# Performance work log

Hardware: AMD Instinct MI355X
Metric: run time of the kernel (lower is better)

The kernel has to match this reference:

```python
import jax, jax.numpy as jnp
import numpy as np

B, S, D, H = 2, 2048, 1024, 16
HD = D // H  # head dim = 64


def setup_inputs() -> dict:
    key = jax.random.key(0)
    ks = jax.random.split(key, 5)
    scale = 0.02
    x = jax.random.normal(ks[0], (B, S, D), dtype=jnp.float32)
    Wqkv = jax.random.normal(ks[1], (D, 3 * D), dtype=jnp.float32) * scale
    bqkv = jnp.zeros((3 * D,), dtype=jnp.float32)
    Wproj = jax.random.normal(ks[2], (D, D), dtype=jnp.float32) * scale
    bproj = jnp.zeros((D,), dtype=jnp.float32)
    return {"x": x, "Wqkv": Wqkv, "bqkv": bqkv, "Wproj": Wproj, "bproj": bproj}


def reference(x, Wqkv, bqkv, Wproj, bproj):
    # fused QKV projection
    qkv = x @ Wqkv + bqkv                      # [B, S, 3D]
    q, k, v = jnp.split(qkv, 3, axis=-1)       # each [B, S, D]
    # split heads -> [B, H, S, HD]
    def heads(t):
        return t.reshape(B, S, H, HD).transpose(0, 2, 1, 3)
    q, k, v = heads(q), heads(k), heads(v)
    # scaled dot-product attention with causal mask (GPT-2 style)
    scores = jnp.einsum('bhqd,bhkd->bhqk', q, k) / jnp.sqrt(jnp.float32(HD))
    causal = jnp.tril(jnp.ones((S, S), dtype=bool))
    scores = jnp.where(causal, scores, jnp.finfo(scores.dtype).min)
    attn = jax.nn.softmax(scores, axis=-1)      # [B, H, S, S]
    out = jnp.einsum('bhqk,bhkd->bhqd', attn, v)  # [B, H, S, HD]
    out = out.transpose(0, 2, 1, 3).reshape(B, S, D)
    return out @ Wproj + bproj
```

## Files before the change

kernel.cpp:

```cpp
#include <hip/hip_runtime.h>
#include <hip/hip_bf16.h>


typedef __attribute__((ext_vector_type(8))) short short8;
typedef __attribute__((ext_vector_type(4))) float float4v;

#define S_LEN 2048
#define NHEAD 16
#define HDIM  64
#define DMODEL 1024

__device__ __forceinline__ unsigned short f2bf(float f) {
    union { float f; unsigned u; } v; v.f = f;
    unsigned r = v.u + 0x7FFF + ((v.u >> 16) & 1);
    return (unsigned short)(r >> 16);
}

__device__ __forceinline__ unsigned fbits_rn(float f) {
    union { float f; unsigned u; } v; v.f = f;
    return v.u + 0x8000u;
}

__device__ __forceinline__ void async16(const void* g, const void* l) {
    __builtin_amdgcn_global_load_lds(
        (const __attribute__((address_space(1))) unsigned int*)g,
        (__attribute__((address_space(3))) unsigned int*)l, 16, 0, 0);
}

__global__ void f32_to_bf16_v4(const float4* __restrict__ in,
                               ushort4* __restrict__ out, int n4) {
    int i = blockIdx.x * blockDim.x + threadIdx.x;
    if (i < n4) {
        float4 v = in[i];
        ushort4 o;
        o.x = f2bf(v.x); o.y = f2bf(v.y); o.z = f2bf(v.z); o.w = f2bf(v.w);
        out[i] = o;
    }
}

__global__ __launch_bounds__(256) void w_transpose_bf16(
    const float* __restrict__ Wqkv, const float* __restrict__ Wproj,
    unsigned short* __restrict__ outQ, unsigned short* __restrict__ outP) {
    __shared__ float t[64][65];
    const float* in; unsigned short* out; int N, bxl;
    if (blockIdx.x < 48) { in = Wqkv;  out = outQ; N = 3072; bxl = blockIdx.x; }
    else                 { in = Wproj; out = outP; N = 1024; bxl = blockIdx.x - 48; }
    const int K = 1024;
    const int kb = blockIdx.y * 64, nb = bxl * 64;
    const int tid = threadIdx.x;
    const int r0 = tid >> 4, c0 = (tid & 15) * 4;
#pragma unroll
    for (int g = 0; g < 4; g++) {
        float4 v = *(const float4*)(in + (size_t)(kb + g * 16 + r0) * N + nb + c0);
        t[g * 16 + r0][c0 + 0] = v.x; t[g * 16 + r0][c0 + 1] = v.y;
        t[g * 16 + r0][c0 + 2] = v.z; t[g * 16 + r0][c0 + 3] = v.w;
    }
    __syncthreads();
#pragma unroll
    for (int g = 0; g < 4; g++) {
        int n = g * 16 + r0;
        ushort4 o;
        o.x = f2bf(t[c0 + 0][n]); o.y = f2bf(t[c0 + 1][n]);
        o.z = f2bf(t[c0 + 2][n]); o.w = f2bf(t[c0 + 3][n]);
        *(ushort4*)(out + (size_t)(nb + n) * K + kb + c0) = o;
    }
}

__global__ __launch_bounds__(256) void v_transpose_sw(
    const unsigned short* __restrict__ V, unsigned short* __restrict__ Vt) {
    __shared__ unsigned short t[64 * 68];
    const int bh = blockIdx.y;
    const int s0 = blockIdx.x * 64;
    const int tid = threadIdx.x;
    const int r = tid >> 2;
    const int c4 = tid & 3;
    const size_t base = (size_t)bh * S_LEN * HDIM;
    union { uint4 v[2]; unsigned short u[16]; } d;
    const unsigned short* src = V + base + (size_t)(s0 + r) * HDIM + c4 * 16;
    d.v[0] = *(const uint4*)(src);
    d.v[1] = *(const uint4*)(src + 8);
#pragma unroll
    for (int j = 0; j < 16; j++) t[(c4 * 16 + j) * 68 + r] = d.u[j];
    __syncthreads();
    const int h4 = r & 15;
    const unsigned short* pl = t + r * 68 + c4 * 16;
    unsigned short* po = Vt + base + (size_t)r * S_LEN + s0
                         + (((c4 * 4) ^ (h4 & 12)) << 2);
    uint2 ug[4];
#pragma unroll
    for (int i = 0; i < 4; i++)
        ug[i ^ (h4 & 3)] = *(const uint2*)(pl + i * 4);
    uint4 w0; w0.x = ug[0].x; w0.y = ug[0].y; w0.z = ug[1].x; w0.w = ug[1].y;
    uint4 w1; w1.x = ug[2].x; w1.y = ug[2].y; w1.z = ug[3].x; w1.w = ug[3].y;
    *(uint4*)(po) = w0;
    *(uint4*)(po + 8) = w1;
}

#define QSCALE 0.18033688f

__global__ __launch_bounds__(256) void gemm_qkv_kernel(
    const unsigned short* __restrict__ A,
    const unsigned short* __restrict__ Bt,
    const float* __restrict__ bias,
    unsigned short* __restrict__ out_q,
    unsigned short* __restrict__ out_k,
    unsigned short* __restrict__ out_v,
    int M, int N, int K)
{
    __shared__ unsigned short smem[128 * 132];
    unsigned short* As = smem;
    unsigned short* Bs = smem + 128 * 32;

    const int tid  = threadIdx.x;
    const int lane = tid & 63;
    const int wave = tid >> 6;
    const int quad = lane >> 4;
    const int l16  = lane & 15;

    const int m0 = blockIdx.y * 128;
    const int n0 = blockIdx.x * 128;
    const int wm = (wave >> 1) * 64;
    const int wn = (wave & 1) * 64;

    float4v acc[4][4];
#pragma unroll
    for (int i = 0; i < 4; i++)
#pragma unroll
        for (int j = 0; j < 4; j++) acc[i][j] = (float4v){0.f, 0.f, 0.f, 0.f};

    const int srow = lane >> 2;
    const int scol = (lane & 3) * 8;

    for (int k0 = 0; k0 < K; k0 += 32) {
        __syncthreads();
#pragma unroll
        for (int it = 0; it < 2; it++) {
            const int rg = it * 64 + wave * 16;
            async16(A  + (size_t)(m0 + rg + srow) * K + k0 + scol,
                    (const char*)As + rg * 64);
            async16(Bt + (size_t)(n0 + rg + srow) * K + k0 + scol,
                    (const char*)Bs + rg * 64);
        }
        __syncthreads();

        short8 af[4], bf[4];
#pragma unroll
        for (int mt = 0; mt < 4; mt++)
            af[mt] = *(const short8*)(As + (wm + mt * 16 + l16) * 32 + quad * 8);
#pragma unroll
        for (int nt = 0; nt < 4; nt++)
            bf[nt] = *(const short8*)(Bs + (wn + nt * 16 + l16) * 32 + quad * 8);
#pragma unroll
        for (int mt = 0; mt < 4; mt++)
#pragma unroll
            for (int nt = 0; nt < 4; nt++)
                acc[mt][nt] = __builtin_amdgcn_mfma_f32_16x16x32_bf16(
                    af[mt], bf[nt], acc[mt][nt], 0, 0, 0);
    }

    __syncthreads();
#pragma unroll
    for (int nt = 0; nt < 4; nt++) {
        const int col = n0 + wn + nt * 16 + l16;
        const float sc = ((col >> 10) == 0) ? QSCALE : 1.0f;
        const float bia = bias[col] * sc;
        const int cold = (wn + nt * 16 + l16) >> 1;
#pragma unroll
        for (int mt = 0; mt < 4; mt++)
#pragma unroll
            for (int r = 0; r < 4; r++) {
                unsigned fb = fbits_rn(acc[mt][nt][r] * sc + bia);
                unsigned fbp = (unsigned)__shfl_xor((int)fb, 1, 64);
                unsigned pd = (l16 & 1)
                    ? __builtin_amdgcn_perm(fb, fbp, 0x07060302)
                    : __builtin_amdgcn_perm(fbp, fb, 0x07060302);
                const int rowl = wm + mt * 16 + quad * 4 + r;
                *((unsigned*)smem + rowl * 66 + cold) = pd;
            }
    }
    __syncthreads();

#pragma unroll
    for (int ps = 0; ps < 8; ps++) {
        const int row = ps * 16 + (tid >> 4);
        const int pc  = tid & 15;
        const int col0 = pc * 8;
        const int haf = col0 >> 6;
        const int cb = n0 + haf * 64;
        const int part = cb >> 10;
        const int h = (cb & 1023) >> 6;
        const int gr = m0 + row;
        const int b = gr >> 11, s = gr & 2047;
        const size_t bhI = (size_t)(b * NHEAD + h);
        const unsigned short* pl = smem + row * 132 + col0;
        uint2 a = *(const uint2*)(pl);
        uint2 bb = *(const uint2*)(pl + 4);
        uint4 w; w.x = a.x; w.y = a.y; w.z = bb.x; w.w = bb.y;
        unsigned short* po;
        if (part == 1) {
            const int plane = (col0 & 63) >> 5;
            po = out_k + ((bhI * 2 + plane) * S_LEN + s) * 32 + (col0 & 31);
        } else {
            unsigned short* dst = (part == 0) ? out_q : out_v;
            po = dst + (bhI * S_LEN + s) * HDIM + (col0 & 63);
        }
        *(uint4*)po = w;
    }
}

__global__ __launch_bounds__(256) void gemm_proj_kernel(
    const unsigned short* __restrict__ A,
    const unsigned short* __restrict__ Bt,
    const float* __restrict__ bias,
    float* __restrict__ out_f,
    int M, int N, int K)
{
    __shared__ unsigned short smem[(64 + 128) * 32];
    unsigned short* As = smem;
    unsigned short* Bs = smem + 64 * 32;

    const int tid  = threadIdx.x;
    const int lane = tid & 63;
    const int wave = tid >> 6;
    const int quad = lane >> 4;
    const int l16  = lane & 15;

    const int m0 = blockIdx.y * 64;
    const int n0 = blockIdx.x * 128;
    const int wm = (wave >> 1) * 32;
    const int wn = (wave & 1) * 64;

    float4v acc[2][4];
#pragma unroll
    for (int i = 0; i < 2; i++)
#pragma unroll
        for (int j = 0; j < 4; j++) acc[i][j] = (float4v){0.f, 0.f, 0.f, 0.f};

    const int srow = lane >> 2;
    const int scol = (lane & 3) * 8;

    for (int k0 = 0; k0 < K; k0 += 32) {
        __syncthreads();
        async16(A + (size_t)(m0 + wave * 16 + srow) * K + k0 + scol,
                (const char*)As + wave * 1024);
#pragma unroll
        for (int it = 0; it < 2; it++) {
            const int rg = it * 64 + wave * 16;
            async16(Bt + (size_t)(n0 + rg + srow) * K + k0 + scol,
                    (const char*)Bs + rg * 64);
        }
        __syncthreads();

        short8 af[2], bf[4];
#pragma unroll
        for (int mt = 0; mt < 2; mt++)
            af[mt] = *(const short8*)(As + (wm + mt * 16 + l16) * 32 + quad * 8);
#pragma unroll
        for (int nt = 0; nt < 4; nt++)
            bf[nt] = *(const short8*)(Bs + (wn + nt * 16 + l16) * 32 + quad * 8);
#pragma unroll
        for (int mt = 0; mt < 2; mt++)
#pragma unroll
            for (int nt = 0; nt < 4; nt++)
                acc[mt][nt] = __builtin_amdgcn_mfma_f32_16x16x32_bf16(
                    af[mt], bf[nt], acc[mt][nt], 0, 0, 0);
    }

#pragma unroll
    for (int nt = 0; nt < 4; nt++) {
        const int col = n0 + wn + nt * 16 + l16;
        const float bia = bias[col];
#pragma unroll
        for (int mt = 0; mt < 2; mt++) {
            const int rowb = m0 + wm + mt * 16 + quad * 4;
#pragma unroll
            for (int r = 0; r < 4; r++)
                out_f[(size_t)(rowb + r) * N + col] = acc[mt][nt][r] + bia;
        }
    }
}

__device__ __forceinline__ void attn_stage(
    const unsigned short* __restrict__ K2, const unsigned short* __restrict__ Vt,
    unsigned short* __restrict__ Ks, unsigned short* __restrict__ Vs,
    size_t baseK, size_t baseV, int kb0, int wave, int lane)
{
#pragma unroll
    for (int it = 0; it < 2; it++)
        async16(K2 + baseK + ((size_t)it * S_LEN + kb0 + wave * 16 + (lane >> 2)) * 32
                    + (lane & 3) * 8,
                (const char*)(Ks + (it * 64 + wave * 16) * 32));
#pragma unroll
    for (int it = 0; it < 2; it++)
        async16(Vt + baseV + (size_t)(it * 32 + wave * 8 + (lane >> 3)) * S_LEN
                    + kb0 + (lane & 7) * 8,
                (const char*)(Vs + (it * 32 + wave * 8) * 64));
}

__global__ __launch_bounds__(256) void attn3_kernel(
    const unsigned short* __restrict__ Q,
    const unsigned short* __restrict__ K2,
    const unsigned short* __restrict__ Vt,
    unsigned short* __restrict__ ctx)
{
    __shared__ unsigned short Ks[2][128 * 32];
    __shared__ unsigned short Vs[2][64 * 64];

    const int tid  = threadIdx.x;
    const int lane = tid & 63;
    const int wave = tid >> 6;
    const int quad = lane >> 4;
    const int l16  = lane & 15;

    const int bx = blockIdx.x;
    const int bh = bx & 31;
    const int qb = 31 - (bx >> 5);
    const int q0 = qb * 64 + wave * 16;
    const int nch = qb + 1;

    const size_t baseQ = (size_t)bh * S_LEN * HDIM;
    const size_t baseK = (size_t)bh * 2 * S_LEN * 32;
    const size_t baseV = (size_t)bh * HDIM * S_LEN;

    short8 qf[2];
#pragma unroll
    for (int h = 0; h < 2; h++)
        qf[h] = *(const short8*)(Q + baseQ + (size_t)(q0 + l16) * HDIM
                                 + h * 32 + quad * 8);

    float4v o[4];
#pragma unroll
    for (int nt = 0; nt < 4; nt++) o[nt] = (float4v){0.f, 0.f, 0.f, 0.f};
    float lsum = 0.f;

    attn_stage(K2, Vt, Ks[0], Vs[0], baseK, baseV, 0, wave, lane);

    for (int c = 0; c < nch; c++) {
        const int buf = c & 1;
        __syncthreads();
        if (c + 1 < nch)
            attn_stage(K2, Vt, Ks[buf ^ 1], Vs[buf ^ 1],
                       baseK, baseV, (c + 1) * 64, wave, lane);

        const int kb0 = c * 64;
        short8 kf[4][2];
#pragma unroll
        for (int kt = 0; kt < 4; kt++)
#pragma unroll
            for (int h = 0; h < 2; h++)
                kf[kt][h] = *(const short8*)&Ks[buf][(h * 64 + kt * 16 + l16) * 32
                                                     + quad * 8];
        float4v st[4];
#pragma unroll
        for (int kt = 0; kt < 4; kt++) {
            st[kt] = __builtin_amdgcn_mfma_f32_16x16x32_bf16(
                kf[kt][0], qf[0], (float4v){0.f, 0.f, 0.f, 0.f}, 0, 0, 0);
            st[kt] = __builtin_amdgcn_mfma_f32_16x16x32_bf16(
                kf[kt][1], qf[1], st[kt], 0, 0, 0);
        }
        const bool lastc = (c == nch - 1);
        const int qpos = q0 + l16;
        float p[4][4];
#pragma unroll
        for (int kt = 0; kt < 4; kt++)
#pragma unroll
            for (int r = 0; r < 4; r++) {
                float x = st[kt][r];
                if (lastc) {
                    int kpos = kb0 + kt * 16 + quad * 4 + r;
                    x = (kpos <= qpos) ? x : -1e30f;
                }
                p[kt][r] = __builtin_amdgcn_exp2f(x);
                lsum += p[kt][r];
            }

        unsigned pk[4][2];
#pragma unroll
        for (int kt = 0; kt < 4; kt++)
#pragma unroll
            for (int j = 0; j < 2; j++)
                pk[kt][j] = __builtin_amdgcn_perm(
                    fbits_rn(p[kt][2 * j + 1]), fbits_rn(p[kt][2 * j]),
                    0x07060302);
        union { unsigned u[4]; short8 s; } pf[2];
#pragma unroll
        for (int kk = 0; kk < 2; kk++)
#pragma unroll
            for (int pp = 0; pp < 4; pp++)
                pf[kk].u[pp] = pk[kk * 2 + (pp >> 1)][pp & 1];

#pragma unroll
        for (int nt = 0; nt < 4; nt++) {
            union { ushort4 h[2]; short8 s; } vf[2];
#pragma unroll
            for (int kt = 0; kt < 4; kt++)
                vf[kt >> 1].h[kt & 1] = *(const ushort4*)&Vs[buf][
                    (nt * 16 + l16) * 64 + (((kt * 4 + quad) ^ l16) << 2)];
            o[nt] = __builtin_amdgcn_mfma_f32_16x16x32_bf16(
                pf[0].s, vf[0].s, o[nt], 0, 0, 0);
            o[nt] = __builtin_amdgcn_mfma_f32_16x16x32_bf16(
                pf[1].s, vf[1].s, o[nt], 0, 0, 0);
        }
    }

    float l = lsum;
    l += __shfl_xor(l, 16, 64);
    l += __shfl_xor(l, 32, 64);
    const float linv = 1.f / l;
    float lr[4];
#pragma unroll
    for (int r = 0; r < 4; r++) lr[r] = __shfl(linv, quad * 4 + r, 64);

    const int b = bh >> 4, h = bh & 15;
#pragma unroll
    for (int r = 0; r < 4; r++) {
        const int s = q0 + quad * 4 + r;
        const size_t off = ((size_t)(b * S_LEN + s)) * DMODEL + h * HDIM;
#pragma unroll
        for (int nt = 0; nt < 4; nt++)
            ctx[off + nt * 16 + l16] = f2bf(o[nt][r] * lr[r]);
    }
}

extern "C" void kernel_launch(void* const* d_in, const int* in_sizes, int n_in,
                              void* d_out, int out_size, void* d_ws, size_t ws_size,
                              hipStream_t stream) {
    const float* x     = (const float*)d_in[0];
    const float* Wqkv  = (const float*)d_in[1];
    const float* bqkv  = (const float*)d_in[2];
    const float* Wproj = (const float*)d_in[3];
    const float* bproj = (const float*)d_in[4];
    float* out = (float*)d_out;

    const int M  = 2 * S_LEN;
    const int N1 = 3 * DMODEL;
    const int K  = DMODEL;

    unsigned short* x_bf    = (unsigned short*)d_ws;
    unsigned short* wqkv_t  = x_bf   + (size_t)M * K;
    unsigned short* wproj_t = wqkv_t + (size_t)K * N1;
    unsigned short* q_bf    = wproj_t + (size_t)K * DMODEL;
    unsigned short* k_bf    = q_bf   + (size_t)M * DMODEL;
    unsigned short* v_bf    = k_bf   + (size_t)M * DMODEL;
    unsigned short* ctx_bf  = v_bf   + (size_t)M * DMODEL;
    unsigned short* vt_bf   = x_bf;

    {
        int n4 = (M * K) / 4;
        f32_to_bf16_v4<<<n4 / 256, 256, 0, stream>>>((const float4*)x,
                                                     (ushort4*)x_bf, n4);
    }
    {
        dim3 g(64, 16);
        w_transpose_bf16<<<g, 256, 0, stream>>>(Wqkv, Wproj, wqkv_t, wproj_t);
    }

    dim3 g1(N1 / 128, M / 128);
    gemm_qkv_kernel<<<g1, 256, 0, stream>>>(x_bf, wqkv_t, bqkv,
                                            q_bf, k_bf, v_bf, M, N1, K);

    {
        dim3 g(S_LEN / 64, 2 * NHEAD);
        v_transpose_sw<<<g, 256, 0, stream>>>(v_bf, vt_bf);
    }

    attn3_kernel<<<1024, 256, 0, stream>>>(q_bf, k_bf, vt_bf, ctx_bf);

    dim3 g3(DMODEL / 128, M / 64);
    gemm_proj_kernel<<<g3, 256, 0, stream>>>(ctx_bf, wproj_t, bproj, out,
                                             M, DMODEL, K);
}
```

Baseline: 195.6 us.

## Deepen GEMM K-step to 64 and enlarge attention query blocks to 128

Both GEMM kernels now load two 32-wide K slices per barrier pair, so each iteration runs twice as many MFMAs between syncs and the number of synchronisations is halved. The attention kernel moves to 512-thread blocks covering 128 query rows, with 8 waves sharing each K/V tile. The query-block order is rescheduled to alternate heavy and light blocks, and causal masking is applied to any chunk overlapping the diagonal rather than only the last one. This aims to cut barrier overhead and increase K/V reuse per load, at the cost of more LDS per GEMM block and fewer, larger attention blocks.

```diff
diff --git a/kernel.cpp b/kernel.cpp
--- a/kernel.cpp
+++ b/kernel.cpp
@@ -109,7 +109,7 @@
 {
     __shared__ unsigned short smem[128 * 132];
     unsigned short* As = smem;
-    unsigned short* Bs = smem + 128 * 32;
+    unsigned short* Bs = smem + 8192;
 
     const int tid  = threadIdx.x;
     const int lane = tid & 63;
@@ -131,31 +131,38 @@
     const int srow = lane >> 2;
     const int scol = (lane & 3) * 8;
 
-    for (int k0 = 0; k0 < K; k0 += 32) {
+    for (int k0 = 0; k0 < K; k0 += 64) {
         __syncthreads();
 #pragma unroll
-        for (int it = 0; it < 2; it++) {
-            const int rg = it * 64 + wave * 16;
-            async16(A  + (size_t)(m0 + rg + srow) * K + k0 + scol,
-                    (const char*)As + rg * 64);
-            async16(Bt + (size_t)(n0 + rg + srow) * K + k0 + scol,
-                    (const char*)Bs + rg * 64);
-        }
+        for (int kk = 0; kk < 2; kk++)
+#pragma unroll
+            for (int it = 0; it < 2; it++) {
+                const int rg = it * 64 + wave * 16;
+                async16(A  + (size_t)(m0 + rg + srow) * K + k0 + kk * 32 + scol,
+                        (const char*)(As + kk * 4096) + rg * 64);
+                async16(Bt + (size_t)(n0 + rg + srow) * K + k0 + kk * 32 + scol,
+                        (const char*)(Bs + kk * 4096) + rg * 64);
+            }
         __syncthreads();
 
-        short8 af[4], bf[4];
-#pragma unroll
-        for (int mt = 0; mt < 4; mt++)
-            af[mt] = *(const short8*)(As + (wm + mt * 16 + l16) * 32 + quad * 8);
-#pragma unroll
-        for (int nt = 0; nt < 4; nt++)
-            bf[nt] = *(const short8*)(Bs + (wn + nt * 16 + l16) * 32 + quad * 8);
-#pragma unroll
-        for (int mt = 0; mt < 4; mt++)
+#pragma unroll
+        for (int kk = 0; kk < 2; kk++) {
+            short8 af[4], bf[4];
+#pragma unroll
+            for (int mt = 0; mt < 4; mt++)
+                af[mt] = *(const short8*)(As + kk * 4096
+                                          + (wm + mt * 16 + l16) * 32 + quad * 8);
 #pragma unroll
             for (int nt = 0; nt < 4; nt++)
-                acc[mt][nt] = __builtin_amdgcn_mfma_f32_16x16x32_bf16(
-                    af[mt], bf[nt], acc[mt][nt], 0, 0, 0);
+                bf[nt] = *(const short8*)(Bs + kk * 4096
+                                          + (wn + nt * 16 + l16) * 32 + quad * 8);
+#pragma unroll
+            for (int mt = 0; mt < 4; mt++)
+#pragma unroll
+                for (int nt = 0; nt < 4; nt++)
+                    acc[mt][nt] = __builtin_amdgcn_mfma_f32_16x16x32_bf16(
+                        af[mt], bf[nt], acc[mt][nt], 0, 0, 0);
+        }
     }
 
     __syncthreads();
@@ -215,9 +222,9 @@
     float* __restrict__ out_f,
     int M, int N, int K)
 {
-    __shared__ unsigned short smem[(64 + 128) * 32];
+    __shared__ unsigned short smem[12288];
     unsigned short* As = smem;
-    unsigned short* Bs = smem + 64 * 32;
+    unsigned short* Bs = smem + 4096;
 
     const int tid  = threadIdx.x;
     const int lane = tid & 63;
@@ -239,31 +246,39 @@
     const int srow = lane >> 2;
     const int scol = (lane & 3) * 8;
 
-    for (int k0 = 0; k0 < K; k0 += 32) {
+    for (int k0 = 0; k0 < K; k0 += 64) {
         __syncthreads();
-        async16(A + (size_t)(m0 + wave * 16 + srow) * K + k0 + scol,
-                (const char*)As + wave * 1024);
-#pragma unroll
-        for (int it = 0; it < 2; it++) {
-            const int rg = it * 64 + wave * 16;
-            async16(Bt + (size_t)(n0 + rg + srow) * K + k0 + scol,
-                    (const char*)Bs + rg * 64);
+#pragma unroll
+        for (int kk = 0; kk < 2; kk++) {
+            async16(A + (size_t)(m0 + wave * 16 + srow) * K + k0 + kk * 32 + scol,
+                    (const char*)(As + kk * 2048) + wave * 1024);
+#pragma unroll
+            for (int it = 0; it < 2; it++) {
+                const int rg = it * 64 + wave * 16;
+                async16(Bt + (size_t)(n0 + rg + srow) * K + k0 + kk * 32 + scol,
+                        (const char*)(Bs + kk * 4096) + rg * 64);
+            }
         }
         __syncthreads();
 
-        short8 af[2], bf[4];
-#pragma unroll
-        for (int mt = 0; mt < 2; mt++)
-            af[mt] = *(const short8*)(As + (wm + mt * 16 + l16) * 32 + quad * 8);
-#pragma unroll
-        for (int nt = 0; nt < 4; nt++)
-            bf[nt] = *(const short8*)(Bs + (wn + nt * 16 + l16) * 32 + quad * 8);
-#pragma unroll
-        for (int mt = 0; mt < 2; mt++)
+#pragma unroll
+        for (int kk = 0; kk < 2; kk++) {
+            short8 af[2], bf[4];
+#pragma unroll
+            for (int mt = 0; mt < 2; mt++)
+                af[mt] = *(const short8*)(As + kk * 2048
+                                          + (wm + mt * 16 + l16) * 32 + quad * 8);
 #pragma unroll
             for (int nt = 0; nt < 4; nt++)
-                acc[mt][nt] = __builtin_amdgcn_mfma_f32_16x16x32_bf16(
-                    af[mt], bf[nt], acc[mt][nt], 0, 0, 0);
+                bf[nt] = *(const short8*)(Bs + kk * 4096
+                                          + (wn + nt * 16 + l16) * 32 + quad * 8);
+#pragma unroll
+            for (int mt = 0; mt < 2; mt++)
+#pragma unroll
+                for (int nt = 0; nt < 4; nt++)
+                    acc[mt][nt] = __builtin_amdgcn_mfma_f32_16x16x32_bf16(
+                        af[mt], bf[nt], acc[mt][nt], 0, 0, 0);
+        }
     }
 
 #pragma unroll
@@ -280,24 +295,7 @@
     }
 }
 
-__device__ __forceinline__ void attn_stage(
-    const unsigned short* __restrict__ K2, const unsigned short* __restrict__ Vt,
-    unsigned short* __restrict__ Ks, unsigned short* __restrict__ Vs,
-    size_t baseK, size_t baseV, int kb0, int wave, int lane)
-{
-#pragma unroll
-    for (int it = 0; it < 2; it++)
-        async16(K2 + baseK + ((size_t)it * S_LEN + kb0 + wave * 16 + (lane >> 2)) * 32
-                    + (lane & 3) * 8,
-                (const char*)(Ks + (it * 64 + wave * 16) * 32));
-#pragma unroll
-    for (int it = 0; it < 2; it++)
-        async16(Vt + baseV + (size_t)(it * 32 + wave * 8 + (lane >> 3)) * S_LEN
-                    + kb0 + (lane & 7) * 8,
-                (const char*)(Vs + (it * 32 + wave * 8) * 64));
-}
-
-__global__ __launch_bounds__(256) void attn3_kernel(
+__global__ __launch_bounds__(512) void attn4_kernel(
     const unsigned short* __restrict__ Q,
     const unsigned short* __restrict__ K2,
     const unsigned short* __restrict__ Vt,
@@ -314,14 +312,20 @@
 
     const int bx = blockIdx.x;
     const int bh = bx & 31;
-    const int qb = 31 - (bx >> 5);
-    const int q0 = qb * 64 + wave * 16;
-    const int nch = qb + 1;
+    const int j  = bx >> 5;
+    const int qb = (j < 8) ? (15 - j) : (j - 8);
+    const int q0 = qb * 128 + wave * 16;
+    const int nch = 2 * qb + 2;
 
     const size_t baseQ = (size_t)bh * S_LEN * HDIM;
     const size_t baseK = (size_t)bh * 2 * S_LEN * 32;
     const size_t baseV = (size_t)bh * HDIM * S_LEN;
 
+    const int krw = wave * 16 + (lane >> 2);
+    const int kcol = (lane & 3) * 8;
+    const int vrw = wave * 8 + (lane >> 3);
+    const int vcol = (lane & 7) * 8;
+
     short8 qf[2];
 #pragma unroll
     for (int h = 0; h < 2; h++)
@@ -333,14 +337,21 @@
     for (int nt = 0; nt < 4; nt++) o[nt] = (float4v){0.f, 0.f, 0.f, 0.f};
     float lsum = 0.f;
 
-    attn_stage(K2, Vt, Ks[0], Vs[0], baseK, baseV, 0, wave, lane);
+#define ATTN_STAGE(buf, kb0)                                                   \
+    do {                                                                       \
+        async16(K2 + baseK + ((size_t)(krw >> 6) * S_LEN + (kb0) + (krw & 63)) \
+                    * 32 + kcol,                                               \
+                (const char*)Ks[buf] + wave * 1024);                           \
+        async16(Vt + baseV + (size_t)vrw * S_LEN + (kb0) + vcol,               \
+                (const char*)Vs[buf] + wave * 1024);                           \
+    } while (0)
+
+    ATTN_STAGE(0, 0);
 
     for (int c = 0; c < nch; c++) {
         const int buf = c & 1;
         __syncthreads();
-        if (c + 1 < nch)
-            attn_stage(K2, Vt, Ks[buf ^ 1], Vs[buf ^ 1],
-                       baseK, baseV, (c + 1) * 64, wave, lane);
+        if (c + 1 < nch) ATTN_STAGE(buf ^ 1, (c + 1) * 64);
 
         const int kb0 = c * 64;
         short8 kf[4][2];
@@ -358,7 +369,7 @@
             st[kt] = __builtin_amdgcn_mfma_f32_16x16x32_bf16(
                 kf[kt][1], qf[1], st[kt], 0, 0, 0);
         }
-        const bool lastc = (c == nch - 1);
+        const bool needm = (kb0 + 63 > q0);
         const int qpos = q0 + l16;
         float p[4][4];
 #pragma unroll
@@ -366,7 +377,7 @@
 #pragma unroll
             for (int r = 0; r < 4; r++) {
                 float x = st[kt][r];
-                if (lastc) {
+                if (needm) {
                     int kpos = kb0 + kt * 16 + quad * 4 + r;
                     x = (kpos <= qpos) ? x : -1e30f;
                 }
@@ -378,9 +389,9 @@
 #pragma unroll
         for (int kt = 0; kt < 4; kt++)
 #pragma unroll
-            for (int j = 0; j < 2; j++)
-                pk[kt][j] = __builtin_amdgcn_perm(
-                    fbits_rn(p[kt][2 * j + 1]), fbits_rn(p[kt][2 * j]),
+            for (int jj = 0; jj < 2; jj++)
+                pk[kt][jj] = __builtin_amdgcn_perm(
+                    fbits_rn(p[kt][2 * jj + 1]), fbits_rn(p[kt][2 * jj]),
                     0x07060302);
         union { unsigned u[4]; short8 s; } pf[2];
 #pragma unroll
@@ -402,6 +413,7 @@
                 pf[1].s, vf[1].s, o[nt], 0, 0, 0);
         }
     }
+#undef ATTN_STAGE
 
     float l = lsum;
     l += __shfl_xor(l, 16, 64);
@@ -464,7 +476,7 @@
         v_transpose_sw<<<g, 256, 0, stream>>>(v_bf, vt_bf);
     }
 
-    attn3_kernel<<<1024, 256, 0, stream>>>(q_bf, k_bf, vt_bf, ctx_bf);
+    attn4_kernel<<<512, 512, 0, stream>>>(q_bf, k_bf, vt_bf, ctx_bf);
 
     dim3 g3(DMODEL / 128, M / 64);
     gemm_proj_kernel<<<g3, 256, 0, stream>>>(ctx_bf, wproj_t, bproj, out,
```

New measurement: 202.5 us. 1.04x slower.
